# Performance work log

Measured on AMD Instinct MI355X. Metric: run time of the kernel, lower is better.

Reference implementation:

```python
import jax, jax.numpy as jnp
import numpy as np

NUM_NODES = 1_000_000
HID = 256
OUT = 128


def _sage_layer(h, src, dst, n_dst, W_self, W_neigh, b):
    # DGL SAGEConv('mean'): mean-aggregate neighbor msgs, then fc_neigh + fc_self + bias
    msgs = h[src]                                                  # [E, F] gather
    sums = jax.ops.segment_sum(msgs, dst, num_segments=n_dst)      # [n_dst, F]
    deg = jax.ops.segment_sum(jnp.ones((src.shape[0],), h.dtype), dst, num_segments=n_dst)
    mean = sums / jnp.maximum(deg, 1.0)[:, None]                   # zero-degree -> 0
    h_self = h[:n_dst]                                             # DGL block: dst = first n_dst src
    return h_self @ W_self + mean @ W_neigh + b


def setup_inputs() -> dict:
    key = jax.random.key(0)
    ks = jax.random.split(key, 12)
    N0, N1, N2 = 1_048_576, 65_536, 4_096
    E0, E1 = 1_048_576, 65_536
    inp = {
        "input_nodes": jax.random.randint(ks[0], (N0,), 0, NUM_NODES),
        "src0": jax.random.randint(ks[1], (E0,), 0, N0),
        "dst0": jax.random.randint(ks[2], (E0,), 0, N1),
        "src1": jax.random.randint(ks[3], (E1,), 0, N1),
        "dst1": jax.random.randint(ks[4], (E1,), 0, N2),
        "n_dst0": N1,
        "n_dst1": N2,
        "embed_table": jax.random.normal(ks[5], (NUM_NODES, HID), jnp.float32),
        "W_self0": jax.random.normal(ks[6], (HID, HID), jnp.float32) / np.sqrt(HID),
        "W_neigh0": jax.random.normal(ks[7], (HID, HID), jnp.float32) / np.sqrt(HID),
        "b0": jnp.zeros((HID,), jnp.float32),
        "W_self1": jax.random.normal(ks[8], (HID, OUT), jnp.float32) / np.sqrt(HID),
        "W_neigh1": jax.random.normal(ks[9], (HID, OUT), jnp.float32) / np.sqrt(HID),
        "b1": jnp.zeros((OUT,), jnp.float32),
    }
    return inp


def reference(input_nodes, src0, dst0, src1, dst1, n_dst0, n_dst1,
              embed_table, W_self0, W_neigh0, b0, W_self1, W_neigh1, b1):
    h = embed_table[input_nodes]                       # [N0, HID] embedding lookup
    h = _sage_layer(h, src0, dst0, n_dst0, W_self0, W_neigh0, b0)
    h = jax.nn.relu(h)                                 # dropout is identity in eval mode
    h = _sage_layer(h, src1, dst1, n_dst1, W_self1, W_neigh1, b1)
    return h                                           # [4096, OUT]
```

## Files before the change

### kernel.cpp

```cpp
#include <hip/hip_runtime.h>
#include <hip/hip_bf16.h>
#include <cstddef>
#include <cstdint>


#define HID 256
#define N1 65536
#define N2 4096

using f32x4  = __attribute__((ext_vector_type(4))) float;
using bf16x8 = __attribute__((ext_vector_type(8))) short;
using u16x8  = __attribute__((ext_vector_type(8))) unsigned short;

static __device__ __forceinline__ ushort f2bf(float f) {
    union { float f; unsigned u; } v; v.f = f;
    unsigned r = v.u + 0x7FFF + ((v.u >> 16) & 1);
    return (ushort)(r >> 16);
}
static __device__ __forceinline__ float bf2f(ushort h) {
    union { unsigned u; float f; } v; v.u = ((unsigned)h) << 16;
    return v.f;
}

__global__ __launch_bounds__(256) void build_wt01(
    const float* __restrict__ Ws0, const float* __restrict__ Wn0,
    const float* __restrict__ Ws1, const float* __restrict__ Wn1,
    ushort* __restrict__ WT0, ushort* __restrict__ WT1)
{
    int i = blockIdx.x * 256 + threadIdx.x;
    if (i < 256 * 512) {
        int n = i >> 9, k = i & 511;
        float v = (k < HID) ? Ws0[(size_t)k * 256 + n] : Wn0[(size_t)(k - HID) * 256 + n];
        WT0[i] = f2bf(v);
    } else {
        int j = i - 256 * 512;
        int n = j >> 9, k = j & 511;
        float v = (k < HID) ? Ws1[(size_t)k * 128 + n] : Wn1[(size_t)(k - HID) * 128 + n];
        WT1[j] = f2bf(v);
    }
}

__global__ __launch_bounds__(256) void edge_hist01(
    const int* __restrict__ dst0, const int* __restrict__ dst1,
    int* __restrict__ cnt01, int E0, int E1)
{
    int i = blockIdx.x * 256 + threadIdx.x;
    if (i < E0) atomicAdd(&cnt01[dst0[i]], 1);
    else if (i < E0 + E1) atomicAdd(&cnt01[N1 + dst1[i - E0]], 1);
}

__global__ __launch_bounds__(256) void scan_block(
    const int* __restrict__ cnt, int* __restrict__ offs, int* __restrict__ totals)
{
    __shared__ int sh[256];
    int t = threadIdx.x;
    int i = blockIdx.x * 256 + t;
    int v = cnt[i];
    sh[t] = v;
    __syncthreads();
    #pragma unroll
    for (int d = 1; d < 256; d <<= 1) {
        int x = (t >= d) ? sh[t - d] : 0;
        __syncthreads();
        sh[t] += x;
        __syncthreads();
    }
    offs[i] = sh[t] - v;
    if (t == 255) totals[blockIdx.x] = sh[t];
}

__global__ __launch_bounds__(512) void scan_totals(
    int* __restrict__ totals, int nb)
{
    __shared__ int sh[512];
    int t = threadIdx.x;
    int v = (t < nb) ? totals[t] : 0;
    sh[t] = v;
    __syncthreads();
    #pragma unroll
    for (int d = 1; d < 512; d <<= 1) {
        int x = (t >= d) ? sh[t - d] : 0;
        __syncthreads();
        sh[t] += x;
        __syncthreads();
    }
    if (t < nb) totals[t] = sh[t] - v;
}

__global__ __launch_bounds__(256) void scan_add(
    int* __restrict__ offs, const int* __restrict__ totals,
    int* __restrict__ cursor, int n, int total_edges)
{
    int i = blockIdx.x * 256 + threadIdx.x;
    if (i < n) {
        int v = offs[i] + totals[i >> 8];
        offs[i] = v;
        cursor[i] = v;
    }
    if (i == 0) offs[n] = total_edges;
}

__global__ __launch_bounds__(256) void edge_scatter01(
    const int* __restrict__ src0, const int* __restrict__ dst0,
    const int* __restrict__ src1, const int* __restrict__ dst1,
    const int* __restrict__ node_idx,
    int* __restrict__ cursor, int* __restrict__ edge_rows, int E0, int E1)
{
    int i = blockIdx.x * 256 + threadIdx.x;
    if (i < E0) {
        int pos = atomicAdd(&cursor[dst0[i]], 1);
        edge_rows[pos] = node_idx[src0[i]];
    } else if (i < E0 + E1) {
        int e = i - E0;
        int pos = atomicAdd(&cursor[N1 + dst1[e]], 1);
        edge_rows[pos] = src1[e];
    }
}

template<bool SRC_F32>
__global__ __launch_bounds__(256) void sage_gather_mean(
    const void* __restrict__ table,
    const int* __restrict__ offs,
    const int* __restrict__ edge_rows,
    ushort* __restrict__ mean_out,
    int n_dst)
{
    int w = blockIdx.x * 4 + (threadIdx.x >> 6);
    int lane = threadIdx.x & 63;
    if (w >= n_dst) return;
    int beg = offs[w], end = offs[w + 1];
    float a0 = 0.f, a1 = 0.f, a2 = 0.f, a3 = 0.f;
    int e = beg;
    while (e < end) {
        int cnt = end - e; cnt = cnt > 8 ? 8 : cnt;
        int myrow = 0;
        if (lane < cnt) myrow = edge_rows[e + lane];
        f32x4  vf[8];
        ushort4 vh[8];
        #pragma unroll
        for (int j = 0; j < 8; ++j) {
            if (j < cnt) {
                int r = __shfl(myrow, j);
                if (SRC_F32)
                    vf[j] = *((const f32x4*)((const float*)table + (size_t)r * HID) + lane);
                else
                    vh[j] = *((const ushort4*)((const ushort*)table + (size_t)r * HID) + lane);
            }
        }
        #pragma unroll
        for (int j = 0; j < 8; ++j) {
            if (j < cnt) {
                if (SRC_F32) { a0 += vf[j].x; a1 += vf[j].y; a2 += vf[j].z; a3 += vf[j].w; }
                else { a0 += bf2f(vh[j].x); a1 += bf2f(vh[j].y); a2 += bf2f(vh[j].z); a3 += bf2f(vh[j].w); }
            }
        }
        e += cnt;
    }
    float inv = 1.0f / (float)max(end - beg, 1);
    ushort4 o;
    o.x = f2bf(a0 * inv); o.y = f2bf(a1 * inv);
    o.z = f2bf(a2 * inv); o.w = f2bf(a3 * inv);
    *((ushort4*)(mean_out + (size_t)w * HID) + lane) = o;
}

template<int BN, bool RELU, bool GATHER, bool SELF_F32, bool OUT_BF16>
__global__ __launch_bounds__(256) void sage_gemm_mfma(
    const void* __restrict__ Aself,
    const int* __restrict__ idx,
    const ushort* __restrict__ Amean,
    const ushort* __restrict__ WT,
    const float* __restrict__ bias,
    void* __restrict__ Out)
{
    constexpr int BM = 64, BK = 64;
    constexpr int WN = BN / 64;
    constexpr int WM = 4 / WN;
    constexpr int M_FR = (BM / WM) / 16;

    __shared__ __align__(16) ushort As[BM * BK];
    __shared__ __align__(16) ushort Bs[BN * BK];

    const int t = threadIdx.x;
    const int brow = blockIdx.x * BM;
    const int w = t >> 6, l = t & 63;
    const int wc = (w % WN) * 64;
    const int wr = (w / WN) * (BM / WM);
    const int l15 = l & 15, l4 = l >> 4;

    f32x4 acc[M_FR][4] = {};
    f32x4 af[4];
    u16x8 ah[2];
    u16x8 bh[BN / 32];

    auto load_step = [&](int k0) {
        if (SELF_F32 && k0 < HID) {
            #pragma unroll
            for (int i = 0; i < 4; ++i) {
                int li = t + i * 256; int r = li >> 4; int k4 = (li & 15) << 2;
                size_t rg = GATHER ? (size_t)idx[brow + r] : (size_t)(brow + r);
                af[i] = *(const f32x4*)((const float*)Aself + rg * HID + k0 + k4);
            }
        } else {
            #pragma unroll
            for (int i = 0; i < 2; ++i) {
                int li = t + i * 256; int r = li >> 3; int k8 = (li & 7) << 3;
                const ushort* sp;
                if (k0 < HID) {
                    size_t rg = GATHER ? (size_t)idx[brow + r] : (size_t)(brow + r);
                    sp = (const ushort*)Aself + rg * HID + k0 + k8;
                } else {
                    sp = Amean + (size_t)(brow + r) * HID + (k0 - HID) + k8;
                }
                ah[i] = *(const u16x8*)sp;
            }
        }
        #pragma unroll
        for (int i = 0; i < BN / 32; ++i) {
            int li = t + i * 256; int n = li >> 3; int k8 = (li & 7) << 3;
            bh[i] = *(const u16x8*)(WT + (size_t)n * 512 + k0 + k8);
        }
    };

    auto store_step = [&](int k0) {
        if (SELF_F32 && k0 < HID) {
            #pragma unroll
            for (int i = 0; i < 4; ++i) {
                int li = t + i * 256; int r = li >> 4; int k4 = (li & 15) << 2;
                ushort4 h;
                h.x = f2bf(af[i].x); h.y = f2bf(af[i].y);
                h.z = f2bf(af[i].z); h.w = f2bf(af[i].w);
                *(ushort4*)&As[(r * BK + k4) ^ ((r & 7) << 3)] = h;
            }
        } else {
            #pragma unroll
            for (int i = 0; i < 2; ++i) {
                int li = t + i * 256; int r = li >> 3; int k8 = (li & 7) << 3;
                *(u16x8*)&As[(r * BK + k8) ^ ((r & 7) << 3)] = ah[i];
            }
        }
        #pragma unroll
        for (int i = 0; i < BN / 32; ++i) {
            int li = t + i * 256; int n = li >> 3; int k8 = (li & 7) << 3;
            *(u16x8*)&Bs[(n * BK + k8) ^ ((n & 7) << 3)] = bh[i];
        }
    };

    load_step(0);
    store_step(0);
    __syncthreads();

    for (int k0 = 0; k0 < 2 * HID; k0 += BK) {
        int kn = k0 + BK;
        if (kn < 2 * HID) load_step(kn);

        #pragma unroll
        for (int kk = 0; kk < 2; ++kk) {
            int koff = kk * 32 + l4 * 8;
            bf16x8 a[M_FR], b[4];
            #pragma unroll
            for (int m = 0; m < M_FR; ++m) {
                int r = wr + m * 16 + l15;
                a[m] = *(const bf16x8*)&As[(r * BK + koff) ^ ((r & 7) << 3)];
            }
            #pragma unroll
            for (int n = 0; n < 4; ++n) {
                int c = wc + n * 16 + l15;
                b[n] = *(const bf16x8*)&Bs[(c * BK + koff) ^ ((c & 7) << 3)];
            }
            #pragma unroll
            for (int m = 0; m < M_FR; ++m)
                #pragma unroll
                for (int n = 0; n < 4; ++n)
                    acc[m][n] = __builtin_amdgcn_mfma_f32_16x16x32_bf16(
                        a[m], b[n], acc[m][n], 0, 0, 0);
        }
        __syncthreads();
        if (kn < 2 * HID) store_step(kn);
        __syncthreads();
    }

    #pragma unroll
    for (int m = 0; m < M_FR; ++m) {
        #pragma unroll
        for (int n = 0; n < 4; ++n) {
            int col = wc + n * 16 + l15;
            float bv = bias[col];
            #pragma unroll
            for (int r = 0; r < 4; ++r) {
                int row = brow + wr + m * 16 + l4 * 4 + r;
                float v = acc[m][n][r] + bv;
                if (RELU) v = fmaxf(v, 0.f);
                if (OUT_BF16) ((ushort*)Out)[(size_t)row * BN + col] = f2bf(v);
                else          ((float*)Out)[(size_t)row * BN + col] = v;
            }
        }
    }
}

extern "C" void kernel_launch(void* const* d_in, const int* in_sizes, int n_in,
                              void* d_out, int out_size, void* d_ws, size_t ws_size,
                              hipStream_t stream) {
    const int*   input_nodes = (const int*)d_in[0];
    const int*   src0        = (const int*)d_in[1];
    const int*   dst0        = (const int*)d_in[2];
    const int*   src1        = (const int*)d_in[3];
    const int*   dst1        = (const int*)d_in[4];
    const float* embed       = (const float*)d_in[7];
    const float* W_self0     = (const float*)d_in[8];
    const float* W_neigh0    = (const float*)d_in[9];
    const float* b0          = (const float*)d_in[10];
    const float* W_self1     = (const float*)d_in[11];
    const float* W_neigh1    = (const float*)d_in[12];
    const float* b1          = (const float*)d_in[13];
    float*       out         = (float*)d_out;

    const int E0 = in_sizes[1];
    const int E1 = in_sizes[3];
    const int NC = N1 + N2;

    char* ws = (char*)d_ws;
    ushort* mean0   = (ushort*)(ws + ((size_t)0  << 20));
    ushort* h1      = (ushort*)(ws + ((size_t)32 << 20));
    int*    edges01 = (int*)  (ws + ((size_t)64 << 20));
    int*    cnt01   = (int*)  (ws + ((size_t)70 << 20));
    int*    tot01   = cnt01 + NC;
    int*    offs01  = (int*)  (ws + ((size_t)71 << 20));
    ushort* WT0     = (ushort*)(ws + ((size_t)72 << 20));
    ushort* WT1     = (ushort*)(ws + ((size_t)73 << 20));
    ushort* mean1   = (ushort*)(ws + ((size_t)74 << 20));

    hipMemsetAsync(cnt01, 0, (size_t)(NC + 272) * 4, stream);
    build_wt01<<<768, 256, 0, stream>>>(W_self0, W_neigh0, W_self1, W_neigh1, WT0, WT1);
    edge_hist01<<<(E0 + E1 + 255) / 256, 256, 0, stream>>>(dst0, dst1, cnt01, E0, E1);
    scan_block<<<NC / 256, 256, 0, stream>>>(cnt01, offs01, tot01);
    scan_totals<<<1, 512, 0, stream>>>(tot01, NC / 256);
    scan_add<<<NC / 256, 256, 0, stream>>>(offs01, tot01, cnt01, NC, E0 + E1);
    edge_scatter01<<<(E0 + E1 + 255) / 256, 256, 0, stream>>>(
        src0, dst0, src1, dst1, input_nodes, cnt01, edges01, E0, E1);

    sage_gather_mean<true><<<N1 / 4, 256, 0, stream>>>(
        embed, offs01, edges01, mean0, N1);
    sage_gemm_mfma<256, true, true, true, true><<<N1 / 64, 256, 0, stream>>>(
        embed, input_nodes, mean0, WT0, b0, h1);

    sage_gather_mean<false><<<N2 / 4, 256, 0, stream>>>(
        h1, offs01 + N1, edges01, mean1, N2);
    sage_gemm_mfma<128, false, false, false, false><<<N2 / 64, 256, 0, stream>>>(
        h1, nullptr, mean1, WT1, b1, out);
}
```

Before: 340.0 us.

## Fuse neighbor mean gather into GEMM kernel and collapse CSR scan into one kernel

Each GEMM block now computes the neighbor means for its 64 destination rows and keeps them in shared memory, so the bf16 mean buffer is no longer written to and re-read from global memory and two launches go away. The three-kernel scan becomes a single 1024-thread block scan, and the memset is folded into the weight-prep kernel. The cost is about 32KB of extra LDS per block, which lowers occupancy. The gather inside the GEMM runs serially per wave before the MFMA loop starts, so there is less latency hiding. Layer 1 has only 64 blocks, each doing 16 rows per wave.

```diff
diff --git a/kernel.cpp b/kernel.cpp
--- a/kernel.cpp
+++ b/kernel.cpp
@@ -7,6 +7,7 @@
 #define HID 256
 #define N1 65536
 #define N2 4096
+#define NC (N1 + N2)
 
 using f32x4  = __attribute__((ext_vector_type(4))) float;
 using bf16x8 = __attribute__((ext_vector_type(8))) short;
@@ -22,12 +23,14 @@
     return v.f;
 }
 
-__global__ __launch_bounds__(256) void build_wt01(
+__global__ __launch_bounds__(256) void prep(
     const float* __restrict__ Ws0, const float* __restrict__ Wn0,
     const float* __restrict__ Ws1, const float* __restrict__ Wn1,
-    ushort* __restrict__ WT0, ushort* __restrict__ WT1)
+    ushort* __restrict__ WT0, ushort* __restrict__ WT1,
+    int* __restrict__ cnt01)
 {
     int i = blockIdx.x * 256 + threadIdx.x;
+    if (i < NC) cnt01[i] = 0;
     if (i < 256 * 512) {
         int n = i >> 9, k = i & 511;
         float v = (k < HID) ? Ws0[(size_t)k * 256 + n] : Wn0[(size_t)(k - HID) * 256 + n];
@@ -49,55 +52,44 @@
     else if (i < E0 + E1) atomicAdd(&cnt01[N1 + dst1[i - E0]], 1);
 }
 
-__global__ __launch_bounds__(256) void scan_block(
-    const int* __restrict__ cnt, int* __restrict__ offs, int* __restrict__ totals)
-{
-    __shared__ int sh[256];
-    int t = threadIdx.x;
-    int i = blockIdx.x * 256 + t;
-    int v = cnt[i];
-    sh[t] = v;
-    __syncthreads();
+__global__ __launch_bounds__(1024) void scan_csr(
+    int* __restrict__ cnt, int* __restrict__ offs)
+{
+    __shared__ int wsum[16];
+    const int t = threadIdx.x;
+    const int lane = t & 63, wid = t >> 6;
+    int carry = 0;
     #pragma unroll
-    for (int d = 1; d < 256; d <<= 1) {
-        int x = (t >= d) ? sh[t - d] : 0;
+    for (int p = 0; p < NC / 4096; ++p) {
+        int4 v = ((const int4*)cnt)[p * 1024 + t];
+        int tsum = v.x + v.y + v.z + v.w;
+        int inc = tsum;
+        #pragma unroll
+        for (int d = 1; d < 64; d <<= 1) {
+            int y = __shfl_up(inc, (unsigned)d, 64);
+            if (lane >= d) inc += y;
+        }
+        if (lane == 63) wsum[wid] = inc;
         __syncthreads();
-        sh[t] += x;
+        int wbase = 0, tot = 0;
+        #pragma unroll
+        for (int j = 0; j < 16; ++j) {
+            int s = wsum[j];
+            if (j < wid) wbase += s;
+            tot += s;
+        }
+        int excl = carry + wbase + (inc - tsum);
+        int4 o;
+        o.x = excl;
+        o.y = o.x + v.x;
+        o.z = o.y + v.y;
+        o.w = o.z + v.z;
+        ((int4*)offs)[p * 1024 + t] = o;
+        ((int4*)cnt)[p * 1024 + t] = o;
+        carry += tot;
         __syncthreads();
     }
-    offs[i] = sh[t] - v;
-    if (t == 255) totals[blockIdx.x] = sh[t];
-}
-
-__global__ __launch_bounds__(512) void scan_totals(
-    int* __restrict__ totals, int nb)
-{
-    __shared__ int sh[512];
-    int t = threadIdx.x;
-    int v = (t < nb) ? totals[t] : 0;
-    sh[t] = v;
-    __syncthreads();
-    #pragma unroll
-    for (int d = 1; d < 512; d <<= 1) {
-        int x = (t >= d) ? sh[t - d] : 0;
-        __syncthreads();
-        sh[t] += x;
-        __syncthreads();
-    }
-    if (t < nb) totals[t] = sh[t] - v;
-}
-
-__global__ __launch_bounds__(256) void scan_add(
-    int* __restrict__ offs, const int* __restrict__ totals,
-    int* __restrict__ cursor, int n, int total_edges)
-{
-    int i = blockIdx.x * 256 + threadIdx.x;
-    if (i < n) {
-        int v = offs[i] + totals[i >> 8];
-        offs[i] = v;
-        cursor[i] = v;
-    }
-    if (i == 0) offs[n] = total_edges;
+    if (t == 0) offs[NC] = carry;
 }
 
 __global__ __launch_bounds__(256) void edge_scatter01(
@@ -117,57 +109,12 @@
     }
 }
 
-template<bool SRC_F32>
-__global__ __launch_bounds__(256) void sage_gather_mean(
+template<int BN, bool RELU, bool GATHER, bool SELF_F32, bool OUT_BF16>
+__global__ __launch_bounds__(256) void sage_fused(
     const void* __restrict__ table,
+    const int* __restrict__ idx,
     const int* __restrict__ offs,
     const int* __restrict__ edge_rows,
-    ushort* __restrict__ mean_out,
-    int n_dst)
-{
-    int w = blockIdx.x * 4 + (threadIdx.x >> 6);
-    int lane = threadIdx.x & 63;
-    if (w >= n_dst) return;
-    int beg = offs[w], end = offs[w + 1];
-    float a0 = 0.f, a1 = 0.f, a2 = 0.f, a3 = 0.f;
-    int e = beg;
-    while (e < end) {
-        int cnt = end - e; cnt = cnt > 8 ? 8 : cnt;
-        int myrow = 0;
-        if (lane < cnt) myrow = edge_rows[e + lane];
-        f32x4  vf[8];
-        ushort4 vh[8];
-        #pragma unroll
-        for (int j = 0; j < 8; ++j) {
-            if (j < cnt) {
-                int r = __shfl(myrow, j);
-                if (SRC_F32)
-                    vf[j] = *((const f32x4*)((const float*)table + (size_t)r * HID) + lane);
-                else
-                    vh[j] = *((const ushort4*)((const ushort*)table + (size_t)r * HID) + lane);
-            }
-        }
-        #pragma unroll
-        for (int j = 0; j < 8; ++j) {
-            if (j < cnt) {
-                if (SRC_F32) { a0 += vf[j].x; a1 += vf[j].y; a2 += vf[j].z; a3 += vf[j].w; }
-                else { a0 += bf2f(vh[j].x); a1 += bf2f(vh[j].y); a2 += bf2f(vh[j].z); a3 += bf2f(vh[j].w); }
-            }
-        }
-        e += cnt;
-    }
-    float inv = 1.0f / (float)max(end - beg, 1);
-    ushort4 o;
-    o.x = f2bf(a0 * inv); o.y = f2bf(a1 * inv);
-    o.z = f2bf(a2 * inv); o.w = f2bf(a3 * inv);
-    *((ushort4*)(mean_out + (size_t)w * HID) + lane) = o;
-}
-
-template<int BN, bool RELU, bool GATHER, bool SELF_F32, bool OUT_BF16>
-__global__ __launch_bounds__(256) void sage_gemm_mfma(
-    const void* __restrict__ Aself,
-    const int* __restrict__ idx,
-    const ushort* __restrict__ Amean,
     const ushort* __restrict__ WT,
     const float* __restrict__ bias,
     void* __restrict__ Out)
@@ -179,6 +126,7 @@
 
     __shared__ __align__(16) ushort As[BM * BK];
     __shared__ __align__(16) ushort Bs[BN * BK];
+    __shared__ __align__(16) ushort meanS[4][BM * BK];
 
     const int t = threadIdx.x;
     const int brow = blockIdx.x * BM;
@@ -193,25 +141,21 @@
     u16x8 bh[BN / 32];
 
     auto load_step = [&](int k0) {
-        if (SELF_F32 && k0 < HID) {
-            #pragma unroll
-            for (int i = 0; i < 4; ++i) {
-                int li = t + i * 256; int r = li >> 4; int k4 = (li & 15) << 2;
-                size_t rg = GATHER ? (size_t)idx[brow + r] : (size_t)(brow + r);
-                af[i] = *(const f32x4*)((const float*)Aself + rg * HID + k0 + k4);
-            }
-        } else {
-            #pragma unroll
-            for (int i = 0; i < 2; ++i) {
-                int li = t + i * 256; int r = li >> 3; int k8 = (li & 7) << 3;
-                const ushort* sp;
-                if (k0 < HID) {
+        if (k0 < HID) {
+            if (SELF_F32) {
+                #pragma unroll
+                for (int i = 0; i < 4; ++i) {
+                    int li = t + i * 256; int r = li >> 4; int k4 = (li & 15) << 2;
                     size_t rg = GATHER ? (size_t)idx[brow + r] : (size_t)(brow + r);
-                    sp = (const ushort*)Aself + rg * HID + k0 + k8;
-                } else {
-                    sp = Amean + (size_t)(brow + r) * HID + (k0 - HID) + k8;
-                }
-                ah[i] = *(const u16x8*)sp;
+                    af[i] = *(const f32x4*)((const float*)table + rg * HID + k0 + k4);
+                }
+            } else {
+                #pragma unroll
+                for (int i = 0; i < 2; ++i) {
+                    int li = t + i * 256; int r = li >> 3; int k8 = (li & 7) << 3;
+                    size_t rg = GATHER ? (size_t)idx[brow + r] : (size_t)(brow + r);
+                    ah[i] = *(const u16x8*)((const ushort*)table + rg * HID + k0 + k8);
+                }
             }
         }
         #pragma unroll
@@ -222,20 +166,22 @@
     };
 
     auto store_step = [&](int k0) {
-        if (SELF_F32 && k0 < HID) {
-            #pragma unroll
-            for (int i = 0; i < 4; ++i) {
-                int li = t + i * 256; int r = li >> 4; int k4 = (li & 15) << 2;
-                ushort4 h;
-                h.x = f2bf(af[i].x); h.y = f2bf(af[i].y);
-                h.z = f2bf(af[i].z); h.w = f2bf(af[i].w);
-                *(ushort4*)&As[(r * BK + k4) ^ ((r & 7) << 3)] = h;
-            }
-        } else {
-            #pragma unroll
-            for (int i = 0; i < 2; ++i) {
-                int li = t + i * 256; int r = li >> 3; int k8 = (li & 7) << 3;
-                *(u16x8*)&As[(r * BK + k8) ^ ((r & 7) << 3)] = ah[i];
+        if (k0 < HID) {
+            if (SELF_F32) {
+                #pragma unroll
+                for (int i = 0; i < 4; ++i) {
+                    int li = t + i * 256; int r = li >> 4; int k4 = (li & 15) << 2;
+                    ushort4 h;
+                    h.x = f2bf(af[i].x); h.y = f2bf(af[i].y);
+                    h.z = f2bf(af[i].z); h.w = f2bf(af[i].w);
+                    *(ushort4*)&As[(r * BK + k4) ^ ((r & 7) << 3)] = h;
+                }
+            } else {
+                #pragma unroll
+                for (int i = 0; i < 2; ++i) {
+                    int li = t + i * 256; int r = li >> 3; int k8 = (li & 7) << 3;
+                    *(u16x8*)&As[(r * BK + k8) ^ ((r & 7) << 3)] = ah[i];
+                }
             }
         }
         #pragma unroll
@@ -246,6 +192,45 @@
     };
 
     load_step(0);
+
+    for (int i = 0; i < 16; ++i) {
+        int row = w * 16 + i;
+        int beg = offs[brow + row], end = offs[brow + row + 1];
+        float a0 = 0.f, a1 = 0.f, a2 = 0.f, a3 = 0.f;
+        int e = beg;
+        while (e < end) {
+            int cnt = end - e; cnt = cnt > 8 ? 8 : cnt;
+            int myrow = 0;
+            if (l < cnt) myrow = edge_rows[e + l];
+            f32x4  vf[8];
+            ushort4 vh[8];
+            #pragma unroll
+            for (int j = 0; j < 8; ++j) {
+                if (j < cnt) {
+                    int r = __shfl(myrow, j);
+                    if (SELF_F32)
+                        vf[j] = *((const f32x4*)((const float*)table + (size_t)r * HID) + l);
+                    else
+                        vh[j] = *((const ushort4*)((const ushort*)table + (size_t)r * HID) + l);
+                }
+            }
+            #pragma unroll
+            for (int j = 0; j < 8; ++j) {
+                if (j < cnt) {
+                    if (SELF_F32) { a0 += vf[j].x; a1 += vf[j].y; a2 += vf[j].z; a3 += vf[j].w; }
+                    else { a0 += bf2f(vh[j].x); a1 += bf2f(vh[j].y); a2 += bf2f(vh[j].z); a3 += bf2f(vh[j].w); }
+                }
+            }
+            e += cnt;
+        }
+        float inv = 1.0f / (float)max(end - beg, 1);
+        ushort4 o;
+        o.x = f2bf(a0 * inv); o.y = f2bf(a1 * inv);
+        o.z = f2bf(a2 * inv); o.w = f2bf(a3 * inv);
+        *(ushort4*)&meanS[l4][(row * BK + l15 * 4) ^ ((row & 7) << 3)] = o;
+    }
+    __syncthreads();
+
     store_step(0);
     __syncthreads();
 
@@ -253,6 +238,7 @@
         int kn = k0 + BK;
         if (kn < 2 * HID) load_step(kn);
 
+        const ushort* abase = (k0 < HID) ? As : meanS[(k0 - HID) >> 6];
         #pragma unroll
         for (int kk = 0; kk < 2; ++kk) {
             int koff = kk * 32 + l4 * 8;
@@ -260,7 +246,7 @@
             #pragma unroll
             for (int m = 0; m < M_FR; ++m) {
                 int r = wr + m * 16 + l15;
-                a[m] = *(const bf16x8*)&As[(r * BK + koff) ^ ((r & 7) << 3)];
+                a[m] = *(const bf16x8*)&abase[(r * BK + koff) ^ ((r & 7) << 3)];
             }
             #pragma unroll
             for (int n = 0; n < 4; ++n) {
@@ -316,35 +302,25 @@
 
     const int E0 = in_sizes[1];
     const int E1 = in_sizes[3];
-    const int NC = N1 + N2;
 
     char* ws = (char*)d_ws;
-    ushort* mean0   = (ushort*)(ws + ((size_t)0  << 20));
-    ushort* h1      = (ushort*)(ws + ((size_t)32 << 20));
-    int*    edges01 = (int*)  (ws + ((size_t)64 << 20));
-    int*    cnt01   = (int*)  (ws + ((size_t)70 << 20));
-    int*    tot01   = cnt01 + NC;
-    int*    offs01  = (int*)  (ws + ((size_t)71 << 20));
-    ushort* WT0     = (ushort*)(ws + ((size_t)72 << 20));
-    ushort* WT1     = (ushort*)(ws + ((size_t)73 << 20));
-    ushort* mean1   = (ushort*)(ws + ((size_t)74 << 20));
-
-    hipMemsetAsync(cnt01, 0, (size_t)(NC + 272) * 4, stream);
-    build_wt01<<<768, 256, 0, stream>>>(W_self0, W_neigh0, W_self1, W_neigh1, WT0, WT1);
+    ushort* h1      = (ushort*)(ws + ((size_t)0  << 20));
+    int*    edges01 = (int*)  (ws + ((size_t)32 << 20));
+    int*    cnt01   = (int*)  (ws + ((size_t)40 << 20));
+    int*    offs01  = (int*)  (ws + ((size_t)41 << 20));
+    ushort* WT0     = (ushort*)(ws + ((size_t)42 << 20));
+    ushort* WT1     = (ushort*)(ws + ((size_t)43 << 20));
+
+    prep<<<768, 256, 0, stream>>>(W_self0, W_neigh0, W_self1, W_neigh1,
+                                  WT0, WT1, cnt01);
     edge_hist01<<<(E0 + E1 + 255) / 256, 256, 0, stream>>>(dst0, dst1, cnt01, E0, E1);
-    scan_block<<<NC / 256, 256, 0, stream>>>(cnt01, offs01, tot01);
-    scan_totals<<<1, 512, 0, stream>>>(tot01, NC / 256);
-    scan_add<<<NC / 256, 256, 0, stream>>>(offs01, tot01, cnt01, NC, E0 + E1);
+    scan_csr<<<1, 1024, 0, stream>>>(cnt01, offs01);
     edge_scatter01<<<(E0 + E1 + 255) / 256, 256, 0, stream>>>(
         src0, dst0, src1, dst1, input_nodes, cnt01, edges01, E0, E1);
 
-    sage_gather_mean<true><<<N1 / 4, 256, 0, stream>>>(
-        embed, offs01, edges01, mean0, N1);
-    sage_gemm_mfma<256, true, true, true, true><<<N1 / 64, 256, 0, stream>>>(
-        embed, input_nodes, mean0, WT0, b0, h1);
-
-    sage_gather_mean<false><<<N2 / 4, 256, 0, stream>>>(
-        h1, offs01 + N1, edges01, mean1, N2);
-    sage_gemm_mfma<128, false, false, false, false><<<N2 / 64, 256, 0, stream>>>(
-        h1, nullptr, mean1, WT1, b1, out);
-}
+    sage_fused<256, true, true, true, true><<<N1 / 64, 256, 0, stream>>>(
+        embed, input_nodes, offs01, edges01, WT0, b0, h1);
+
+    sage_fused<128, false, false, false, false><<<N2 / 64, 256, 0, stream>>>(
+        h1, nullptr, offs01 + N1, edges01, WT1, b1, out);
+}
```

After: 617.3 us. +81.5%, slower.
